# Kernel tuning notes

Measured on AMD Instinct MI355X. Metric: run time of the kernel, lower is better.

## Reference

```python
import jax, jax.numpy as jnp
import numpy as np

B, S, N, E = 2048, 5, 80, 592
FX, FF, FE, D = 8, 4, 8, 8
H = 800  # GRU hidden


def setup_inputs() -> dict:
    key = jax.random.key(0)
    ks = jax.random.split(key, 20)
    inp = {
        "x": jax.random.normal(ks[0], (B, S, N, FX), jnp.float32),
        "edge_index": jax.random.randint(ks[1], (B, S, 2, E), 0, N, jnp.int32),
        "edge_f": jax.random.normal(ks[2], (B, S, E, FF), jnp.float32),
        "edge_attr": jax.random.normal(ks[3], (B, S, E, FE), jnp.float32),
        # GNN (net_ResEG) params
        "Wx": jax.random.normal(ks[4], (FX, D), jnp.float32) * 0.1,
        "We": jax.random.normal(ks[5], (FE, D), jnp.float32) * 0.1,
        "Wf": jax.random.normal(ks[6], (FF, D), jnp.float32) * 0.1,
        "Wedge": jax.random.normal(ks[7], (2 * D + FE, D), jnp.float32) * 0.1,
        # GRU params (PyTorch layout: [3H, in])
        "w_ih": jax.random.normal(ks[8], (3 * H, N * D + E * D), jnp.float32) * 0.02,
        "w_hh": jax.random.normal(ks[9], (3 * H, H), jnp.float32) * 0.02,
        "b_ih": jnp.zeros((3 * H,), jnp.float32),
        "b_hh": jnp.zeros((3 * H,), jnp.float32),
        # MLP params
        "mlp_w1": jax.random.normal(ks[10], (S * H, 1280), jnp.float32) * 0.02,
        "mlp_b1": jnp.zeros((1280,), jnp.float32),
        "mlp_w2": jax.random.normal(ks[11], (1280, S * 80), jnp.float32) * 0.02,
        "mlp_b2": jnp.zeros((S * 80,), jnp.float32),
    }
    return inp


def _gnn(xg, eig, efg, eag, Wx, We, Wf, Wedge):
    # one graph: xg [N,FX], eig [2,E], efg [E,FF], eag [E,FE]
    src, dst = eig[0], eig[1]
    m = jax.nn.relu(eag @ We + efg @ Wf)            # [E,D] edge messages
    agg = jnp.zeros((N, D), m.dtype).at[dst].add(m)  # scatter-add to nodes
    x_out = xg + jax.nn.relu(xg @ Wx + agg)          # residual node update [N,D]
    feat = jnp.concatenate([x_out[src], x_out[dst], eag], axis=-1)  # [E,2D+FE]
    e_out = eag + jax.nn.relu(feat @ Wedge)          # residual edge update [E,D]
    return x_out, e_out


def _forward(x, edge_index, edge_f, edge_attr, Wx, We, Wf, Wedge,
             w_ih, w_hh, b_ih, b_hh, mlp_w1, mlp_b1, mlp_w2, mlp_b2):
    # normalize edge indices (edge_index[i,j] - edge_index[i,j,0].min())
    mins = edge_index[:, :, 0, :].min(axis=-1)[:, :, None, None]  # [B,S,1,1]
    ei = edge_index - mins

    flat = lambda a: a.reshape((B * S,) + a.shape[2:])
    x1, e1 = jax.vmap(lambda a, b, c, d: _gnn(a, b, c, d, Wx, We, Wf, Wedge))(
        flat(x), flat(ei), flat(edge_f), flat(edge_attr))
    x1 = x1.reshape(B, S, N * D)
    e1 = e1.reshape(B, S, E * D)
    seq = jnp.concatenate([x1, e1], axis=2)  # [B,S,5376]

    # single-layer GRU, batch_first (dropout inactive for 1 layer)
    def step(h, xt):
        gi = xt @ w_ih.T + b_ih   # [B,3H]
        gh = h @ w_hh.T + b_hh
        ir, iz, inn = jnp.split(gi, 3, axis=-1)
        hr, hz, hn = jnp.split(gh, 3, axis=-1)
        r = jax.nn.sigmoid(ir + hr)
        z = jax.nn.sigmoid(iz + hz)
        n = jnp.tanh(inn + r * hn)
        h_new = (1.0 - z) * n + z * h
        return h_new, h_new

    h0 = jnp.zeros((B, H), seq.dtype)
    _, ys = jax.lax.scan(step, h0, jnp.swapaxes(seq, 0, 1))  # [S,B,H]
    y = jnp.swapaxes(ys, 0, 1).reshape(B, S * H)             # [B,4000]

    y = y @ mlp_w1 + mlp_b1
    y = y @ mlp_w2 + mlp_b2
    return y.reshape(B, 80, 5)


def reference(x, edge_index, edge_f, edge_attr, Wx, We, Wf, Wedge,
              w_ih, w_hh, b_ih, b_hh, mlp_w1, mlp_b1, mlp_w2, mlp_b2):
    return _forward(x, edge_index, edge_f, edge_attr, Wx, We, Wf, Wedge,
                    w_ih, w_hh, b_ih, b_hh, mlp_w1, mlp_b1, mlp_w2, mlp_b2)
```

## Files before the change

kernel.cpp:

```cpp
#include <hip/hip_runtime.h>
#include <math.h>

constexpr int B_  = 2048;
constexpr int S_  = 5;
constexpr int N_  = 80;
constexpr int E_  = 592;
constexpr int FX_ = 8;
constexpr int FF_ = 4;
constexpr int FE_ = 8;
constexpr int D_  = 8;
constexpr int H_  = 800;

constexpr int BS_  = B_ * S_;
constexpr int XD_  = N_ * D_;
constexpr int ED_  = E_ * D_;
constexpr int SEQ_ = XD_ + ED_;
constexpr int G3_  = 3 * H_;
constexpr int MIN_ = S_ * H_;
constexpr int MH_  = 1280;
constexpr int MO_  = S_ * 80;

typedef __bf16 bf16_t;
typedef __bf16 bf16x8 __attribute__((ext_vector_type(8)));
typedef float  f32x4  __attribute__((ext_vector_type(4)));

__device__ __forceinline__ float sigmoidf_(float x) {
    return 1.0f / (1.0f + expf(-x));
}

__device__ __forceinline__ void async16(const void* g, void* l) {
    __builtin_amdgcn_global_load_lds(
        (const __attribute__((address_space(1))) unsigned int*)g,
        (__attribute__((address_space(3))) unsigned int*)l,
        16, 0, 0);
}

__global__ __launch_bounds__(256, 4) void gnn_kernel(
    const float* __restrict__ x,
    const int*   __restrict__ ei,
    const float* __restrict__ ef,
    const float* __restrict__ ea,
    const float* __restrict__ Wx,
    const float* __restrict__ We,
    const float* __restrict__ Wf,
    const float* __restrict__ Wedge,
    bf16_t* __restrict__ seq)
{
    const int tid  = threadIdx.x;
    const int w    = tid >> 6;
    const int lane = tid & 63;
    const int g    = blockIdx.x * 4 + w;

    __shared__ float sWx[FX_ * D_];
    __shared__ float sWe[FE_ * D_];
    __shared__ float sWf[FF_ * D_];
    __shared__ float sWedge[24 * D_];
    __shared__ float agg[4][D_ * N_];
    __shared__ float su [4][D_ * N_];
    __shared__ float sv [4][D_ * N_];

    if (tid < 64) { sWx[tid] = Wx[tid]; sWe[tid] = We[tid]; }
    if (tid < 32) sWf[tid] = Wf[tid];
    if (tid < 192) sWedge[tid] = Wedge[tid];

    float* aggw = agg[w];
    float* uw   = su[w];
    float* vw   = sv[w];
    for (int i = lane; i < D_ * N_; i += 64) aggw[i] = 0.0f;

    const int* srcp = ei + (size_t)g * 2 * E_;
    const int* dstp = srcp + E_;

    int lmin = 0x7fffffff;
    for (int e = lane; e < E_; e += 64) lmin = min(lmin, srcp[e]);
    #pragma unroll
    for (int off = 32; off; off >>= 1)
        lmin = min(lmin, __shfl_xor(lmin, off, 64));
    const int mn = lmin;

    __syncthreads();

    const float* eag = ea + (size_t)g * E_ * FE_;
    const float* efg = ef + (size_t)g * E_ * FF_;
    for (int e = lane; e < E_; e += 64) {
        const float4* ap = (const float4*)(eag + (size_t)e * FE_);
        float4 a0 = ap[0], a1 = ap[1];
        float4 f0 = *(const float4*)(efg + (size_t)e * FF_);
        float a[FE_] = {a0.x, a0.y, a0.z, a0.w, a1.x, a1.y, a1.z, a1.w};
        float fv[FF_] = {f0.x, f0.y, f0.z, f0.w};

        int dadj = dstp[e] - mn;
        if (dadj < 0) dadj += N_;

        #pragma unroll
        for (int d = 0; d < D_; d++) {
            float m = 0.0f;
            #pragma unroll
            for (int k = 0; k < FE_; k++) m += a[k] * sWe[k * D_ + d];
            #pragma unroll
            for (int k = 0; k < FF_; k++) m += fv[k] * sWf[k * D_ + d];
            atomicAdd(&aggw[d * N_ + dadj], fmaxf(m, 0.0f));
        }
    }
    __syncthreads();

    const float* xg = x + (size_t)g * N_ * FX_;
    bf16_t* seqrow = seq + (size_t)g * SEQ_;
    for (int n = lane; n < N_; n += 64) {
        const float4* xp = (const float4*)(xg + (size_t)n * FX_);
        float4 x0 = xp[0], x1 = xp[1];
        float xi[FX_] = {x0.x, x0.y, x0.z, x0.w, x1.x, x1.y, x1.z, x1.w};

        float xo[D_];
        bf16x8 pk;
        #pragma unroll
        for (int d = 0; d < D_; d++) {
            float v = aggw[d * N_ + n];
            #pragma unroll
            for (int k = 0; k < FX_; k++) v += xi[k] * sWx[k * D_ + d];
            xo[d] = xi[d] + fmaxf(v, 0.0f);
            pk[d] = (bf16_t)xo[d];
        }
        *(bf16x8*)(seqrow + (size_t)n * D_) = pk;

        #pragma unroll
        for (int d = 0; d < D_; d++) {
            float uu = 0.0f, vv = 0.0f;
            #pragma unroll
            for (int k = 0; k < D_; k++) {
                uu += xo[k] * sWedge[k * D_ + d];
                vv += xo[k] * sWedge[(D_ + k) * D_ + d];
            }
            uw[d * N_ + n] = uu;
            vw[d * N_ + n] = vv;
        }
    }
    __syncthreads();

    for (int e = lane; e < E_; e += 64) {
        const float4* ap = (const float4*)(eag + (size_t)e * FE_);
        float4 a0 = ap[0], a1 = ap[1];
        float a[FE_] = {a0.x, a0.y, a0.z, a0.w, a1.x, a1.y, a1.z, a1.w};

        int sadj = srcp[e] - mn;
        int dadj = dstp[e] - mn;
        if (dadj < 0) dadj += N_;

        bf16x8 pk;
        #pragma unroll
        for (int d = 0; d < D_; d++) {
            float t = uw[d * N_ + sadj] + vw[d * N_ + dadj];
            #pragma unroll
            for (int k = 0; k < FE_; k++) t += a[k] * sWedge[(2 * D_ + k) * D_ + d];
            pk[d] = (bf16_t)(a[d] + fmaxf(t, 0.0f));
        }
        *(bf16x8*)(seqrow + XD_ + (size_t)e * D_) = pk;
    }
}

template <typename OutT>
__global__ __launch_bounds__(256) void mfma_gemm_bt(
    const bf16_t* __restrict__ A,
    const bf16_t* __restrict__ Bm,
    const float*  __restrict__ bias,
    OutT* __restrict__ C,
    int M, int Nn, int K)
{
    __shared__ bf16_t As[128 * 32];
    __shared__ bf16_t Bs[128 * 32];

    const int tid  = threadIdx.x;
    const int wave = tid >> 6;
    const int lane = tid & 63;
    const int m0 = blockIdx.y * 128;
    const int n0 = blockIdx.x * 128;
    const int wm = (wave & 1) * 64;
    const int wn = (wave >> 1) * 64;

    const int srow  = tid >> 2;
    const int skoff = (tid & 3) * 8;

    const int fm = lane & 15;
    const int fk = (lane >> 4) * 8;

    f32x4 acc[4][4] = {};

    const bf16_t* a_ptr0 = A + (size_t)(m0 + srow) * K + skoff;
    const bf16_t* a_ptr1 = a_ptr0 + (size_t)64 * K;
    int brow0 = n0 + srow;      if (brow0 > Nn - 1) brow0 = Nn - 1;
    int brow1 = n0 + 64 + srow; if (brow1 > Nn - 1) brow1 = Nn - 1;
    const bf16_t* b_ptr0 = Bm + (size_t)brow0 * K + skoff;
    const bf16_t* b_ptr1 = Bm + (size_t)brow1 * K + skoff;

    bf16_t* lA0 = &As[srow * 32 + skoff];
    bf16_t* lA1 = &As[(64 + srow) * 32 + skoff];
    bf16_t* lB0 = &Bs[srow * 32 + skoff];
    bf16_t* lB1 = &Bs[(64 + srow) * 32 + skoff];

    for (int k0 = 0; k0 < K; k0 += 32) {
        async16(a_ptr0 + k0, lA0);
        async16(a_ptr1 + k0, lA1);
        async16(b_ptr0 + k0, lB0);
        async16(b_ptr1 + k0, lB1);
        __syncthreads();

        bf16x8 af[4], bfm[4];
        #pragma unroll
        for (int i = 0; i < 4; i++)
            af[i] = *(const bf16x8*)&As[(wm + i * 16 + fm) * 32 + fk];
        #pragma unroll
        for (int j = 0; j < 4; j++)
            bfm[j] = *(const bf16x8*)&Bs[(wn + j * 16 + fm) * 32 + fk];

        #pragma unroll
        for (int i = 0; i < 4; i++)
            #pragma unroll
            for (int j = 0; j < 4; j++)
                acc[i][j] = __builtin_amdgcn_mfma_f32_16x16x32_bf16(
                    af[i], bfm[j], acc[i][j], 0, 0, 0);

        __syncthreads();
    }

    const int crow = (lane >> 4) * 4;
    const int ccol = lane & 15;
    #pragma unroll
    for (int i = 0; i < 4; i++) {
        #pragma unroll
        for (int j = 0; j < 4; j++) {
            int row = m0 + wm + i * 16 + crow;
            int col = n0 + wn + j * 16 + ccol;
            if (col < Nn) {
                float bv = bias[col];
                #pragma unroll
                for (int r = 0; r < 4; r++) {
                    float v = acc[i][j][r] + bv;
                    C[(size_t)(row + r) * Nn + col] = (OutT)v;
                }
            }
        }
    }
}

__global__ __launch_bounds__(256) void f2bf_kernel(
    const float* __restrict__ in, bf16_t* __restrict__ out, int n)
{
    int i = (blockIdx.x * 256 + threadIdx.x) * 4;
    if (i + 3 < n) {
        float4 v = *(const float4*)&in[i];
        out[i + 0] = (bf16_t)v.x;
        out[i + 1] = (bf16_t)v.y;
        out[i + 2] = (bf16_t)v.z;
        out[i + 3] = (bf16_t)v.w;
    } else {
        for (; i < n; i++) out[i] = (bf16_t)in[i];
    }
}

__global__ __launch_bounds__(256) void tconv_kernel(
    const float* __restrict__ in, bf16_t* __restrict__ out, int K, int N)
{
    __shared__ float tile[32][33];
    int k0 = blockIdx.y * 32, n0 = blockIdx.x * 32;
    int tx = threadIdx.x & 31, ty = threadIdx.x >> 5;
    #pragma unroll
    for (int r = 0; r < 32; r += 8) {
        int k = k0 + ty + r, n = n0 + tx;
        tile[ty + r][tx] = (k < K && n < N) ? in[(size_t)k * N + n] : 0.0f;
    }
    __syncthreads();
    #pragma unroll
    for (int r = 0; r < 32; r += 8) {
        int n = n0 + ty + r, k = k0 + tx;
        if (n < N && k < K) out[(size_t)n * K + k] = (bf16_t)tile[tx][ty + r];
    }
}

__global__ __launch_bounds__(256) void gru_gates_kernel(
    const float* __restrict__ gi,
    const float* __restrict__ gh,
    float*  __restrict__ h,
    bf16_t* __restrict__ hb,
    bf16_t* __restrict__ yb,
    int t)
{
    int i = blockIdx.x * blockDim.x + threadIdx.x;
    if (i >= B_ * H_) return;
    int b = i / H_;
    int j = i - b * H_;
    const float* girow = gi + ((size_t)b * S_ + t) * G3_;
    const float* ghrow = gh + (size_t)b * G3_;
    float r = sigmoidf_(girow[j] + ghrow[j]);
    float z = sigmoidf_(girow[H_ + j] + ghrow[H_ + j]);
    float n = tanhf(girow[2 * H_ + j] + r * ghrow[2 * H_ + j]);
    float hp = h[i];
    float hn = (1.0f - z) * n + z * hp;
    h[i] = hn;
    hb[i] = (bf16_t)hn;
    yb[(size_t)b * MIN_ + t * H_ + j] = (bf16_t)hn;
}

extern "C" void kernel_launch(void* const* d_in, const int* in_sizes, int n_in,
                              void* d_out, int out_size, void* d_ws, size_t ws_size,
                              hipStream_t stream) {
    const float* x     = (const float*)d_in[0];
    const int*   ei    = (const int*)  d_in[1];
    const float* ef    = (const float*)d_in[2];
    const float* ea    = (const float*)d_in[3];
    const float* Wx    = (const float*)d_in[4];
    const float* We    = (const float*)d_in[5];
    const float* Wf    = (const float*)d_in[6];
    const float* Wedge = (const float*)d_in[7];
    const float* w_ih  = (const float*)d_in[8];
    const float* w_hh  = (const float*)d_in[9];
    const float* b_ih  = (const float*)d_in[10];
    const float* b_hh  = (const float*)d_in[11];
    const float* w1    = (const float*)d_in[12];
    const float* b1    = (const float*)d_in[13];
    const float* w2    = (const float*)d_in[14];
    const float* b2    = (const float*)d_in[15];
    float* out = (float*)d_out;

    char* p = (char*)d_ws;
    auto alloc = [&](size_t bytes) {
        void* r = (void*)p;
        p += (bytes + 255) & ~(size_t)255;
        return r;
    };
    bf16_t* seq   = (bf16_t*)alloc((size_t)BS_ * SEQ_ * 2);
    bf16_t* wihb  = (bf16_t*)alloc((size_t)G3_ * SEQ_ * 2);
    bf16_t* whhb  = (bf16_t*)alloc((size_t)G3_ * H_ * 2);
    bf16_t* w1t   = (bf16_t*)alloc((size_t)MH_ * MIN_ * 2);
    bf16_t* w2t   = (bf16_t*)alloc((size_t)MO_ * MH_ * 2);
    float*  gi    = (float*) alloc((size_t)BS_ * G3_ * 4);
    float*  gh    = (float*) alloc((size_t)B_ * G3_ * 4);
    float*  h     = (float*) alloc((size_t)B_ * H_ * 4);
    bf16_t* hb    = (bf16_t*)alloc((size_t)B_ * H_ * 2);
    bf16_t* yb    = (bf16_t*)alloc((size_t)B_ * MIN_ * 2);
    bf16_t* t1b   = (bf16_t*)alloc((size_t)B_ * MH_ * 2);

    hipMemsetAsync(h,  0, (size_t)B_ * H_ * sizeof(float), stream);
    hipMemsetAsync(hb, 0, (size_t)B_ * H_ * sizeof(bf16_t), stream);

    {
        int n = G3_ * SEQ_;
        f2bf_kernel<<<(n / 4 + 255) / 256, 256, 0, stream>>>(w_ih, wihb, n);
    }
    {
        int n = G3_ * H_;
        f2bf_kernel<<<(n / 4 + 255) / 256, 256, 0, stream>>>(w_hh, whhb, n);
    }
    {
        dim3 grid((MH_ + 31) / 32, (MIN_ + 31) / 32);
        tconv_kernel<<<grid, 256, 0, stream>>>(w1, w1t, MIN_, MH_);
    }
    {
        dim3 grid((MO_ + 31) / 32, (MH_ + 31) / 32);
        tconv_kernel<<<grid, 256, 0, stream>>>(w2, w2t, MH_, MO_);
    }

    gnn_kernel<<<BS_ / 4, 256, 0, stream>>>(x, ei, ef, ea, Wx, We, Wf, Wedge, seq);

    {
        dim3 grid((G3_ + 127) / 128, BS_ / 128);
        mfma_gemm_bt<float><<<grid, 256, 0, stream>>>(seq, wihb, b_ih, gi, BS_, G3_, SEQ_);
    }

    for (int t = 0; t < S_; t++) {
        dim3 grid((G3_ + 127) / 128, B_ / 128);
        mfma_gemm_bt<float><<<grid, 256, 0, stream>>>(hb, whhb, b_hh, gh, B_, G3_, H_);
        gru_gates_kernel<<<(B_ * H_ + 255) / 256, 256, 0, stream>>>(gi, gh, h, hb, yb, t);
    }

    {
        dim3 grid((MH_ + 127) / 128, B_ / 128);
        mfma_gemm_bt<bf16_t><<<grid, 256, 0, stream>>>(yb, w1t, b1, t1b, B_, MH_, MIN_);
    }
    {
        dim3 grid((MO_ + 127) / 128, B_ / 128);
        mfma_gemm_bt<float><<<grid, 256, 0, stream>>>(t1b, w2t, b2, out, B_, MO_, MH_);
    }
}
```

Measured before the change: 1.505 ms.

## Add larger-tile double-buffered MFMA GEMM for GRU input projection

Adds a new GEMM kernel with 256x128x64 tiles, 512 threads, XOR-swizzled LDS, async global-to-LDS double buffering, and block-index swizzling for L2 locality. It is used for the large input-projection GEMM (10240x2400x5376), which dominates the runtime. The aim is more data reuse per tile and overlap of loads with MFMA work. In exchange it uses more LDS per block, which can lower occupancy. It also requires M to divide 256 and K to divide 64; 5376/64 = 84, so the shapes here satisfy that.

```diff
diff --git a/kernel.cpp b/kernel.cpp
--- a/kernel.cpp
+++ b/kernel.cpp
@@ -155,6 +155,127 @@
             pk[d] = (bf16_t)(a[d] + fmaxf(t, 0.0f));
         }
         *(bf16x8*)(seqrow + XD_ + (size_t)e * D_) = pk;
+    }
+}
+
+__global__ __launch_bounds__(512, 2) void mfma_gemm_big(
+    const bf16_t* __restrict__ A,
+    const bf16_t* __restrict__ Bm,
+    const float*  __restrict__ bias,
+    float* __restrict__ C,
+    int M, int Nn, int K)
+{
+    constexpr int TBM = 256, TBN = 128, TBK = 64;
+    __shared__ bf16_t As[2][TBM * TBK];
+    __shared__ bf16_t Bs[2][TBN * TBK];
+
+    const int tid  = threadIdx.x;
+    const int wave = tid >> 6;
+    const int lane = tid & 63;
+
+    const int nbx = gridDim.x;
+    const int cpx = nbx >> 3;
+    const int bid = blockIdx.x;
+    const int swz = (bid & 7) * cpx + (bid >> 3);
+    const int ntn = (Nn + TBN - 1) / TBN;
+    const int m0 = (swz / ntn) * TBM;
+    const int n0 = (swz % ntn) * TBN;
+
+    const int wr = wave >> 1;
+    const int wc = wave & 1;
+
+    const int r_loc  = tid >> 3;
+    const int s_slot = tid & 7;
+
+    const int fr = lane & 15;
+    const int fq = lane >> 4;
+
+    f32x4 acc[4][4] = {};
+
+    const int nkt = K / TBK;
+
+    auto STAGE = [&](int t, int buf) {
+        const size_t k0 = (size_t)t * TBK;
+        #pragma unroll
+        for (int i = 0; i < 4; i++) {
+            int row = i * 64 + r_loc;
+            int gsl = s_slot ^ (row & 7);
+            const bf16_t* gp = A + (size_t)(m0 + row) * K + k0 + gsl * 8;
+            async16(gp, &As[buf][row * TBK + s_slot * 8]);
+        }
+        #pragma unroll
+        for (int i = 0; i < 2; i++) {
+            int row = i * 64 + r_loc;
+            int gsl = s_slot ^ (row & 7);
+            int br = n0 + row; if (br > Nn - 1) br = Nn - 1;
+            const bf16_t* gp = Bm + (size_t)br * K + k0 + gsl * 8;
+            async16(gp, &Bs[buf][row * TBK + s_slot * 8]);
+        }
+    };
+
+    STAGE(0, 0);
+    STAGE(nkt > 1 ? 1 : 0, 1);
+    asm volatile("s_waitcnt vmcnt(6)" ::: "memory");
+    __builtin_amdgcn_sched_barrier(0);
+    __builtin_amdgcn_s_barrier();
+
+    for (int t = 0; t < nkt; ++t) {
+        const int c = t & 1;
+        const bf16_t* Ab = As[c];
+        const bf16_t* Bb = Bs[c];
+
+        bf16x8 af[2][4], bfr[2][4];
+        #pragma unroll
+        for (int kk = 0; kk < 2; kk++) {
+            #pragma unroll
+            for (int m = 0; m < 4; m++) {
+                int r = wr * 64 + m * 16 + fr;
+                int g = (kk * 4 + fq) ^ (r & 7);
+                af[kk][m] = *(const bf16x8*)&Ab[r * TBK + g * 8];
+            }
+            #pragma unroll
+            for (int n = 0; n < 4; n++) {
+                int cc = wc * 64 + n * 16 + fr;
+                int g = (kk * 4 + fq) ^ (cc & 7);
+                bfr[kk][n] = *(const bf16x8*)&Bb[cc * TBK + g * 8];
+            }
+        }
+
+        __builtin_amdgcn_s_setprio(1);
+        #pragma unroll
+        for (int kk = 0; kk < 2; kk++)
+            #pragma unroll
+            for (int m = 0; m < 4; m++)
+                #pragma unroll
+                for (int n = 0; n < 4; n++)
+                    acc[m][n] = __builtin_amdgcn_mfma_f32_16x16x32_bf16(
+                        af[kk][m], bfr[kk][n], acc[m][n], 0, 0, 0);
+        __builtin_amdgcn_s_setprio(0);
+
+        __builtin_amdgcn_sched_barrier(0);
+        __builtin_amdgcn_s_barrier();
+
+        int tn = t + 2; if (tn > nkt - 1) tn = nkt - 1;
+        STAGE(tn, c);
+        asm volatile("s_waitcnt vmcnt(6)" ::: "memory");
+        __builtin_amdgcn_sched_barrier(0);
+        __builtin_amdgcn_s_barrier();
+    }
+
+    const int crow = fq * 4;
+    #pragma unroll
+    for (int m = 0; m < 4; m++) {
+        #pragma unroll
+        for (int n = 0; n < 4; n++) {
+            int row = m0 + wr * 64 + m * 16 + crow;
+            int col = n0 + wc * 64 + n * 16 + fr;
+            if (col < Nn) {
+                float bv = bias[col];
+                #pragma unroll
+                for (int r = 0; r < 4; r++)
+                    C[(size_t)(row + r) * Nn + col] = acc[m][n][r] + bv;
+            }
+        }
     }
 }
 
@@ -362,8 +483,8 @@
     gnn_kernel<<<BS_ / 4, 256, 0, stream>>>(x, ei, ef, ea, Wx, We, Wf, Wedge, seq);
 
     {
-        dim3 grid((G3_ + 127) / 128, BS_ / 128);
-        mfma_gemm_bt<float><<<grid, 256, 0, stream>>>(seq, wihb, b_ih, gi, BS_, G3_, SEQ_);
+        int nblocks = (BS_ / 256) * ((G3_ + 127) / 128);
+        mfma_gemm_big<<<nblocks, 512, 0, stream>>>(seq, wihb, b_ih, gi, BS_, G3_, SEQ_);
     }
 
     for (int t = 0; t < S_; t++) {
```

Measured after the change: 1.507 ms. Within noise of the previous version (+0.2%).

## Double-buffer GEMM LDS tiles with XOR swizzle and XCD-aware block remap

Applied to the files above, without the earlier changes.

Replaces the single-buffered MFMA GEMM with a templated kernel that prefetches the next K tile into a second LDS buffer while computing on the current one. LDS rows get an XOR swizzle to cut bank conflicts. Blocks move to a 1D grid with an XCD-aware remap, and the input projection uses a 64-wide K tile. This targets exposed global-load latency and LDS conflicts, at the cost of more LDS per block and possibly lower occupancy.

```diff
diff --git a/kernel.cpp b/kernel.cpp
--- a/kernel.cpp
+++ b/kernel.cpp
@@ -158,83 +158,126 @@
     }
 }
 
-template <typename OutT>
-__global__ __launch_bounds__(256) void mfma_gemm_bt(
+template <int TBK, typename OutT>
+__global__ __launch_bounds__(256) void gemm2ph(
     const bf16_t* __restrict__ A,
     const bf16_t* __restrict__ Bm,
     const float*  __restrict__ bias,
     OutT* __restrict__ C,
     int M, int Nn, int K)
 {
-    __shared__ bf16_t As[128 * 32];
-    __shared__ bf16_t Bs[128 * 32];
+    constexpr int GR  = TBK / 8;
+    constexpr int GM  = GR - 1;
+    constexpr int RPI = 256 / GR;
+    constexpr int NISS = 128 / RPI;
+    constexpr int KK  = TBK / 32;
+
+    __shared__ bf16_t As[2][128 * TBK];
+    __shared__ bf16_t Bs[2][128 * TBK];
 
     const int tid  = threadIdx.x;
     const int wave = tid >> 6;
     const int lane = tid & 63;
-    const int m0 = blockIdx.y * 128;
-    const int n0 = blockIdx.x * 128;
+
+    const int nbx = gridDim.x;
+    int swz = blockIdx.x;
+    if ((nbx & 7) == 0) {
+        int cpx = nbx >> 3;
+        swz = (swz & 7) * cpx + (swz >> 3);
+    }
+    const int ntn = (Nn + 127) >> 7;
+    const int m0 = (swz / ntn) * 128;
+    const int n0 = (swz % ntn) * 128;
+
     const int wm = (wave & 1) * 64;
     const int wn = (wave >> 1) * 64;
 
-    const int srow  = tid >> 2;
-    const int skoff = (tid & 3) * 8;
-
-    const int fm = lane & 15;
-    const int fk = (lane >> 4) * 8;
+    const int r_loc  = tid / GR;
+    const int s_slot = tid % GR;
+
+    const int fr = lane & 15;
+    const int fq = lane >> 4;
 
     f32x4 acc[4][4] = {};
-
-    const bf16_t* a_ptr0 = A + (size_t)(m0 + srow) * K + skoff;
-    const bf16_t* a_ptr1 = a_ptr0 + (size_t)64 * K;
-    int brow0 = n0 + srow;      if (brow0 > Nn - 1) brow0 = Nn - 1;
-    int brow1 = n0 + 64 + srow; if (brow1 > Nn - 1) brow1 = Nn - 1;
-    const bf16_t* b_ptr0 = Bm + (size_t)brow0 * K + skoff;
-    const bf16_t* b_ptr1 = Bm + (size_t)brow1 * K + skoff;
-
-    bf16_t* lA0 = &As[srow * 32 + skoff];
-    bf16_t* lA1 = &As[(64 + srow) * 32 + skoff];
-    bf16_t* lB0 = &Bs[srow * 32 + skoff];
-    bf16_t* lB1 = &Bs[(64 + srow) * 32 + skoff];
-
-    for (int k0 = 0; k0 < K; k0 += 32) {
-        async16(a_ptr0 + k0, lA0);
-        async16(a_ptr1 + k0, lA1);
-        async16(b_ptr0 + k0, lB0);
-        async16(b_ptr1 + k0, lB1);
-        __syncthreads();
-
-        bf16x8 af[4], bfm[4];
-        #pragma unroll
-        for (int i = 0; i < 4; i++)
-            af[i] = *(const bf16x8*)&As[(wm + i * 16 + fm) * 32 + fk];
-        #pragma unroll
-        for (int j = 0; j < 4; j++)
-            bfm[j] = *(const bf16x8*)&Bs[(wn + j * 16 + fm) * 32 + fk];
-
-        #pragma unroll
-        for (int i = 0; i < 4; i++)
-            #pragma unroll
-            for (int j = 0; j < 4; j++)
-                acc[i][j] = __builtin_amdgcn_mfma_f32_16x16x32_bf16(
-                    af[i], bfm[j], acc[i][j], 0, 0, 0);
-
-        __syncthreads();
-    }
-
-    const int crow = (lane >> 4) * 4;
-    const int ccol = lane & 15;
+    const int nkt = K / TBK;
+
+    auto STAGE = [&](int t, int buf) {
+        const size_t k0 = (size_t)t * TBK;
+        #pragma unroll
+        for (int i = 0; i < NISS; i++) {
+            int row = i * RPI + r_loc;
+            int gsl = s_slot ^ (row & GM);
+            async16(A + (size_t)(m0 + row) * K + k0 + gsl * 8,
+                    &As[buf][row * TBK + s_slot * 8]);
+        }
+        #pragma unroll
+        for (int i = 0; i < NISS; i++) {
+            int row = i * RPI + r_loc;
+            int gsl = s_slot ^ (row & GM);
+            int br = n0 + row; if (br > Nn - 1) br = Nn - 1;
+            async16(Bm + (size_t)br * K + k0 + gsl * 8,
+                    &Bs[buf][row * TBK + s_slot * 8]);
+        }
+    };
+
+    STAGE(0, 0);
+    asm volatile("s_waitcnt vmcnt(0)" ::: "memory");
+    __builtin_amdgcn_sched_barrier(0);
+    __builtin_amdgcn_s_barrier();
+
+    for (int t = 0; t < nkt; ++t) {
+        const int c = t & 1;
+        int tn = t + 1; if (tn > nkt - 1) tn = nkt - 1;
+        STAGE(tn, c ^ 1);
+
+        const bf16_t* Ab = As[c];
+        const bf16_t* Bb = Bs[c];
+        bf16x8 af[KK][4], bfr[KK][4];
+        #pragma unroll
+        for (int kk = 0; kk < KK; kk++) {
+            #pragma unroll
+            for (int m = 0; m < 4; m++) {
+                int r = wm + m * 16 + fr;
+                int g = (kk * 4 + fq) ^ (r & GM);
+                af[kk][m] = *(const bf16x8*)&Ab[r * TBK + g * 8];
+            }
+            #pragma unroll
+            for (int n = 0; n < 4; n++) {
+                int cc = wn + n * 16 + fr;
+                int g = (kk * 4 + fq) ^ (cc & GM);
+                bfr[kk][n] = *(const bf16x8*)&Bb[cc * TBK + g * 8];
+            }
+        }
+
+        __builtin_amdgcn_s_setprio(1);
+        #pragma unroll
+        for (int kk = 0; kk < KK; kk++)
+            #pragma unroll
+            for (int m = 0; m < 4; m++)
+                #pragma unroll
+                for (int n = 0; n < 4; n++)
+                    acc[m][n] = __builtin_amdgcn_mfma_f32_16x16x32_bf16(
+                        af[kk][m], bfr[kk][n], acc[m][n], 0, 0, 0);
+        __builtin_amdgcn_s_setprio(0);
+
+        __builtin_amdgcn_sched_barrier(0);
+        asm volatile("s_waitcnt vmcnt(0)" ::: "memory");
+        __builtin_amdgcn_sched_barrier(0);
+        __builtin_amdgcn_s_barrier();
+    }
+
+    const int crow = fq * 4;
     #pragma unroll
-    for (int i = 0; i < 4; i++) {
-        #pragma unroll
-        for (int j = 0; j < 4; j++) {
-            int row = m0 + wm + i * 16 + crow;
-            int col = n0 + wn + j * 16 + ccol;
+    for (int m = 0; m < 4; m++) {
+        #pragma unroll
+        for (int n = 0; n < 4; n++) {
+            int row = m0 + wm + m * 16 + crow;
+            int col = n0 + wn + n * 16 + fr;
             if (col < Nn) {
                 float bv = bias[col];
                 #pragma unroll
                 for (int r = 0; r < 4; r++) {
-                    float v = acc[i][j][r] + bv;
+                    float v = acc[m][n][r] + bv;
                     C[(size_t)(row + r) * Nn + col] = (OutT)v;
                 }
             }
@@ -362,22 +405,22 @@
     gnn_kernel<<<BS_ / 4, 256, 0, stream>>>(x, ei, ef, ea, Wx, We, Wf, Wedge, seq);
 
     {
-        dim3 grid((G3_ + 127) / 128, BS_ / 128);
-        mfma_gemm_bt<float><<<grid, 256, 0, stream>>>(seq, wihb, b_ih, gi, BS_, G3_, SEQ_);
+        int nblocks = (BS_ / 128) * ((G3_ + 127) / 128);
+        gemm2ph<64, float><<<nblocks, 256, 0, stream>>>(seq, wihb, b_ih, gi, BS_, G3_, SEQ_);
     }
 
     for (int t = 0; t < S_; t++) {
-        dim3 grid((G3_ + 127) / 128, B_ / 128);
-        mfma_gemm_bt<float><<<grid, 256, 0, stream>>>(hb, whhb, b_hh, gh, B_, G3_, H_);
+        int nblocks = (B_ / 128) * ((G3_ + 127) / 128);
+        gemm2ph<32, float><<<nblocks, 256, 0, stream>>>(hb, whhb, b_hh, gh, B_, G3_, H_);
         gru_gates_kernel<<<(B_ * H_ + 255) / 256, 256, 0, stream>>>(gi, gh, h, hb, yb, t);
     }
 
     {
-        dim3 grid((MH_ + 127) / 128, B_ / 128);
-        mfma_gemm_bt<bf16_t><<<grid, 256, 0, stream>>>(yb, w1t, b1, t1b, B_, MH_, MIN_);
-    }
-    {
-        dim3 grid((MO_ + 127) / 128, B_ / 128);
-        mfma_gemm_bt<float><<<grid, 256, 0, stream>>>(t1b, w2t, b2, out, B_, MO_, MH_);
-    }
-}
+        int nblocks = (B_ / 128) * ((MH_ + 127) / 128);
+        gemm2ph<32, bf16_t><<<nblocks, 256, 0, stream>>>(yb, w1t, b1, t1b, B_, MH_, MIN_);
+    }
+    {
+        int nblocks = (B_ / 128) * ((MO_ + 127) / 128);
+        gemm2ph<32, float><<<nblocks, 256, 0, stream>>>(t1b, w2t, b2, out, B_, MO_, MH_);
+    }
+}
```

Result: faster. 1.413 ms (-6.1%).
